# Optimization experiments

Hardware: AMD Instinct MI355X
Metric: run time of the kernel (lower is better)

## Reference

```python
import jax, jax.numpy as jnp
import numpy as np

D = 32      # bond_dim
N = 784     # 28*28 physical sites
HALF = 392  # single_rank = rank // 2
L = 10      # labels
B = 128     # batch


def setup_inputs() -> dict:
    key = jax.random.key(0)
    k0, k1, k2, k3, k4, k5 = jax.random.split(key, 6)
    # per-site 2-component input features; components sum to 1 so the
    # 392-step transfer-matrix product stays numerically stable in fp32
    u = jax.random.uniform(k0, (B, N), dtype=jnp.float32)
    x = jnp.stack([u, 1.0 - u], axis=-1)  # (B, 784, 2)

    eye = jnp.eye(D, dtype=jnp.float32)[None, :, None, :]  # (1, D, 1, D)
    a0 = jax.random.normal(k1, (D, 2), dtype=jnp.float32) / np.float32(np.sqrt(D))
    cores_left = eye + 0.01 * jax.random.normal(k2, (HALF - 1, D, 2, D), dtype=jnp.float32)
    core_mid = 0.05 * jax.random.normal(k3, (D, L, D), dtype=jnp.float32)
    cores_right = eye + 0.01 * jax.random.normal(k4, (HALF - 1, D, 2, D), dtype=jnp.float32)
    a_end = jax.random.normal(k5, (D, 2), dtype=jnp.float32) / np.float32(np.sqrt(D))
    return {"x": x, "a0": a0, "cores_left": cores_left, "core_mid": core_mid,
            "cores_right": cores_right, "a_end": a_end}


def reference(x, a0, cores_left, core_mid, cores_right, a_end):
    # ---- left half: nodes 0..391 contracted with inputs 0..391 ----
    v0 = jnp.einsum('dp,bp->bd', a0, x[:, 0])                       # (B, D)
    # input-contracted transfer matrices for nodes 1..391
    Ml = jnp.einsum('nlpr,bnp->nblr', cores_left, x[:, 1:HALF])      # (391, B, D, D)

    def step_left(c, M):
        return jnp.einsum('bl,blr->br', c, M), None

    left, _ = jax.lax.scan(step_left, v0, Ml)                        # (B, D)

    # ---- right half: nodes 393..784 contracted with inputs 392..783 ----
    r0 = jnp.einsum('dp,bp->bd', a_end, x[:, N - 1])                 # (B, D)
    Mr = jnp.einsum('nlpr,bnp->nblr', cores_right, x[:, HALF:N - 1])  # (391, B, D, D)

    def step_right(c, M):
        return jnp.einsum('blr,br->bl', M, c), None

    right, _ = jax.lax.scan(step_right, r0, Mr, reverse=True)        # (B, D)

    # ---- middle label node: original does einsum('a,aba,a->b') (diagonal!) ----
    mid_diag = jnp.einsum('aba->ab', core_mid)                       # (D, L)
    return jnp.einsum('ba,ba,ac->bc', left, right, mid_diag)         # (B, 10)
```

## Files before the change

### kernel.cpp

```cpp
#include <hip/hip_runtime.h>

#define NSTEP 391
#define NB 128

typedef __attribute__((ext_vector_type(8))) short s8v;
typedef __attribute__((ext_vector_type(16))) float f32x16;

typedef const __attribute__((address_space(1))) void* gas_ptr;
typedef __attribute__((address_space(3))) void* las_ptr;

union I4S8 { int4 i; s8v v; };
union W4S8 { int w[4]; s8v v; };

#define WAITVM(N) do { asm volatile("s_waitcnt vmcnt(" #N ")" ::: "memory"); \
                       __builtin_amdgcn_sched_barrier(0); } while (0)
#define LGKM0     do { asm volatile("s_waitcnt lgkmcnt(0)" ::: "memory");   \
                       __builtin_amdgcn_sched_barrier(0); } while (0)
#define SBAR      do { __builtin_amdgcn_s_barrier();                        \
                       __builtin_amdgcn_sched_barrier(0); } while (0)

__device__ __forceinline__ int pack_hi(float a, float b) {
    return (__float_as_int(b) & 0xffff0000) | ((unsigned)__float_as_int(a) >> 16);
}
__device__ __forceinline__ float trunc_bf(float a) {
    return __int_as_float(__float_as_int(a) & 0xffff0000);
}
__device__ __forceinline__ int cvtpk(float a, float b) {
    int r;
    asm("v_cvt_pk_bf16_f32 %0, %1, %2" : "=v"(r) : "v"(a), "v"(b));
    return r;
}

__global__ __launch_bounds__(256) void prep(
    const float* __restrict__ coresL, const float* __restrict__ coresR,
    int* __restrict__ aprep) {
    const int bid = blockIdx.x;
    const int side = bid >= NSTEP;
    const int t = bid - side * NSTEP;
    const float* st = (side ? coresR : coresL) + t * 2048;
    int* out = aprep + (size_t)(side * NSTEP + t) * 2048;
    for (int o = threadIdx.x; o < 2048; o += 256) {
        const int f = o >> 8, lane = (o >> 2) & 63, w = o & 3;
        const int part = f >> 2, p = (f >> 1) & 1, j = f & 1;
        const int h = lane >> 5, c = lane & 31;
        const int k0 = j * 16 + h * 8 + w * 2;
        float e0, e1;
        if (!side) { e0 = st[c * 64 + p * 32 + k0];  e1 = st[c * 64 + p * 32 + k0 + 1]; }
        else       { e0 = st[k0 * 64 + p * 32 + c];  e1 = st[(k0 + 1) * 64 + p * 32 + c]; }
        out[o] = (part == 0) ? pack_hi(e0, e1)
                             : pack_hi(e0 - trunc_bf(e0), e1 - trunc_bf(e1));
    }
}

__device__ __forceinline__ void bpack(const float* d, bool h0, W4S8& b1h, W4S8& b2h,
                                      W4S8& b1l, W4S8& b2l) {
#if __has_builtin(__builtin_amdgcn_permlane32_swap)
    int hw[8], lw[8];
    #pragma unroll
    for (int q = 0; q < 8; ++q) {
        float e = d[2 * q], o = d[2 * q + 1];
        hw[q] = __builtin_amdgcn_perm(__float_as_uint(o), __float_as_uint(e), 0x07060302u);
        lw[q] = cvtpk(e - trunc_bf(e), o - trunc_bf(o));
    }
    {
        auto r0 = __builtin_amdgcn_permlane32_swap(hw[0], hw[2], false, false);
        b1h.w[0] = r0[0]; b1h.w[2] = r0[1];
        auto r1 = __builtin_amdgcn_permlane32_swap(hw[1], hw[3], false, false);
        b1h.w[1] = r1[0]; b1h.w[3] = r1[1];
        auto r2 = __builtin_amdgcn_permlane32_swap(hw[4], hw[6], false, false);
        b2h.w[0] = r2[0]; b2h.w[2] = r2[1];
        auto r3 = __builtin_amdgcn_permlane32_swap(hw[5], hw[7], false, false);
        b2h.w[1] = r3[0]; b2h.w[3] = r3[1];
        auto r4 = __builtin_amdgcn_permlane32_swap(lw[0], lw[2], false, false);
        b1l.w[0] = r4[0]; b1l.w[2] = r4[1];
        auto r5 = __builtin_amdgcn_permlane32_swap(lw[1], lw[3], false, false);
        b1l.w[1] = r5[0]; b1l.w[3] = r5[1];
        auto r6 = __builtin_amdgcn_permlane32_swap(lw[4], lw[6], false, false);
        b2l.w[0] = r6[0]; b2l.w[2] = r6[1];
        auto r7 = __builtin_amdgcn_permlane32_swap(lw[5], lw[7], false, false);
        b2l.w[1] = r7[0]; b2l.w[3] = r7[1];
    }
    (void)h0;
#else
    float sx[16];
    #pragma unroll
    for (int r = 0; r < 16; ++r) sx[r] = __shfl_xor(d[r], 32);
    float B1[8], B2[8];
    #pragma unroll
    for (int m = 0; m < 4; ++m) {
        B1[m]     = h0 ? d[m]      : sx[4 + m];
        B1[4 + m] = h0 ? sx[m]     : d[4 + m];
        B2[m]     = h0 ? d[8 + m]  : sx[12 + m];
        B2[4 + m] = h0 ? sx[8 + m] : d[12 + m];
    }
    #pragma unroll
    for (int ww = 0; ww < 4; ++ww) {
        b1h.w[ww] = pack_hi(B1[2 * ww], B1[2 * ww + 1]);
        b2h.w[ww] = pack_hi(B2[2 * ww], B2[2 * ww + 1]);
        b1l.w[ww] = cvtpk(B1[2 * ww] - trunc_bf(B1[2 * ww]),
                          B1[2 * ww + 1] - trunc_bf(B1[2 * ww + 1]));
        b2l.w[ww] = cvtpk(B2[2 * ww] - trunc_bf(B2[2 * ww]),
                          B2[2 * ww + 1] - trunc_bf(B2[2 * ww + 1]));
    }
#endif
}

__device__ __forceinline__ void mstep(float* d, const I4S8* fr,
                                      const W4S8& b1h, const W4S8& b2h,
                                      const W4S8& b1l, const W4S8& b2l, float2 xv) {
    f32x16 acc0 = {}; f32x16 acc1 = {};
    acc0 = __builtin_amdgcn_mfma_f32_32x32x16_bf16(fr[0].v, b1h.v, acc0, 0, 0, 0);
    acc1 = __builtin_amdgcn_mfma_f32_32x32x16_bf16(fr[2].v, b1h.v, acc1, 0, 0, 0);
    acc0 = __builtin_amdgcn_mfma_f32_32x32x16_bf16(fr[1].v, b2h.v, acc0, 0, 0, 0);
    acc1 = __builtin_amdgcn_mfma_f32_32x32x16_bf16(fr[3].v, b2h.v, acc1, 0, 0, 0);
    acc0 = __builtin_amdgcn_mfma_f32_32x32x16_bf16(fr[0].v, b1l.v, acc0, 0, 0, 0);
    acc1 = __builtin_amdgcn_mfma_f32_32x32x16_bf16(fr[2].v, b1l.v, acc1, 0, 0, 0);
    acc0 = __builtin_amdgcn_mfma_f32_32x32x16_bf16(fr[1].v, b2l.v, acc0, 0, 0, 0);
    acc1 = __builtin_amdgcn_mfma_f32_32x32x16_bf16(fr[3].v, b2l.v, acc1, 0, 0, 0);
    acc0 = __builtin_amdgcn_mfma_f32_32x32x16_bf16(fr[4].v, b1h.v, acc0, 0, 0, 0);
    acc1 = __builtin_amdgcn_mfma_f32_32x32x16_bf16(fr[6].v, b1h.v, acc1, 0, 0, 0);
    acc0 = __builtin_amdgcn_mfma_f32_32x32x16_bf16(fr[5].v, b2h.v, acc0, 0, 0, 0);
    acc1 = __builtin_amdgcn_mfma_f32_32x32x16_bf16(fr[7].v, b2h.v, acc1, 0, 0, 0);
    #pragma unroll
    for (int r = 0; r < 16; ++r) d[r] = fmaf(xv.y, acc1[r], xv.x * acc0[r]);
}

__device__ __forceinline__ void issue_part(const int* tb, int* slot, int lane, int wv) {
    const int f0 = wv * 2;
    __builtin_amdgcn_global_load_lds((gas_ptr)(tb + f0 * 256 + lane * 4),
                                     (las_ptr)(slot + f0 * 256), 16, 0, 0);
    __builtin_amdgcn_global_load_lds((gas_ptr)(tb + (f0 + 1) * 256 + lane * 4),
                                     (las_ptr)(slot + (f0 + 1) * 256), 16, 0, 0);
}

template <int NG>
__global__ __launch_bounds__(256, 4) void stage1(
    const float* __restrict__ x, const int* __restrict__ aprep,
    float* __restrict__ qws) {
    __shared__ int ring[2][2048];
    __shared__ float2 xls[8][16];
    const int wv = threadIdx.x >> 6;
    const int lane = threadIdx.x & 63;
    constexpr int SPX = 2 * NG / 8;
    const int dsp = blockIdx.x;
    const int xcd = dsp & 7;
    const int s = dsp >> 3;
    const int stream = xcd + 8 * (s % SPX);
    const int inb = s / SPX;
    const int side = stream >= NG;
    const int g = stream & (NG - 1);
    const int b0 = inb * 8 + wv * 2;
    constexpr int qq = NSTEP / NG, rr = NSTEP % NG;
    const int a = g * qq + (g < rr ? g : rr);
    const int len = qq + (g < rr ? 1 : 0);
    const int h = lane >> 5, col = lane & 31;
    const bool h0 = (h == 0);

    {
        const int u = lane >> 5, ll = lane & 31;
        if (ll < len) {
            int t = side ? (392 + a + ll) : (a + len - ll);
            xls[wv * 2 + u][ll] = ((const float2*)x + (b0 + u) * 784)[t];
        }
    }

    float dA[16], dB[16];
    #pragma unroll
    for (int r = 0; r < 16; ++r) {
        float iv = (((r & 3) + 8 * (r >> 2) + 4 * h) == col) ? 1.0f : 0.0f;
        dA[r] = iv; dB[r] = iv;
    }

    const int* tbase = aprep + (size_t)side * NSTEP * 2048;
    auto taddr = [&](int j) {
        int t = side ? (a + j) : (a + len - 1 - j);
        t = t < 0 ? 0 : (t > NSTEP - 1 ? NSTEP - 1 : t);
        return tbase + (size_t)t * 2048;
    };

    issue_part(taddr(0), ring[0], lane, wv);
    issue_part(taddr(1), ring[1], lane, wv);

    for (int j = 0; j < len; ++j) {
        int* slot = ring[j & 1];
        W4S8 p1h, p2h, p1l, p2l, q1h, q2h, q1l, q2l;
        bpack(dA, h0, p1h, p2h, p1l, p2l);
        bpack(dB, h0, q1h, q2h, q1l, q2l);
        WAITVM(2);
        SBAR;
        I4S8 fr[8];
        #pragma unroll
        for (int f = 0; f < 8; ++f)
            fr[f].i = *(const int4*)(slot + f * 256 + lane * 4);
        LGKM0;
        SBAR;
        issue_part(taddr(j + 2), slot, lane, wv);
        mstep(dA, fr, p1h, p2h, p1l, p2l, xls[wv * 2][j]);
        mstep(dB, fr, q1h, q2h, q1l, q2l, xls[wv * 2 + 1][j]);
    }
    WAITVM(0);

    float4* q0 = (float4*)(qws + ((size_t)(side * NB + b0) * NG + g) * 1024 + lane * 16);
    float4* q1 = (float4*)(qws + ((size_t)(side * NB + b0 + 1) * NG + g) * 1024 + lane * 16);
    q0[0] = make_float4(dA[0], dA[1], dA[2], dA[3]);
    q0[1] = make_float4(dA[4], dA[5], dA[6], dA[7]);
    q0[2] = make_float4(dA[8], dA[9], dA[10], dA[11]);
    q0[3] = make_float4(dA[12], dA[13], dA[14], dA[15]);
    q1[0] = make_float4(dB[0], dB[1], dB[2], dB[3]);
    q1[1] = make_float4(dB[4], dB[5], dB[6], dB[7]);
    q1[2] = make_float4(dB[8], dB[9], dB[10], dB[11]);
    q1[3] = make_float4(dB[12], dB[13], dB[14], dB[15]);
}

template <int NG>
__global__ __launch_bounds__(64) void stage2f(
    const float* __restrict__ x, const float* __restrict__ a0,
    const float* __restrict__ aend, const float* __restrict__ qws,
    const float* __restrict__ mid, float* __restrict__ out) {
    __shared__ float ring[2][2048];
    const int b = blockIdx.x;
    const int lane = threadIdx.x;
    const int c = lane & 31;
    const int j = lane >> 5;
    const float2* xb = (const float2*)x + b * 784;
    float2 x0 = xb[0], xe = xb[783];
    float v0 = fmaf(a0[c * 2], x0.x, a0[c * 2 + 1] * x0.y);
    float v1 = fmaf(aend[c * 2], xe.x, aend[c * 2 + 1] * xe.y);

    auto issue = [&](int i, float* slot) {
        int ic = i < NG - 1 ? i : NG - 1;
        const float* t0 = qws + ((size_t)b * NG + ic) * 1024;
        const float* t1 = qws + ((size_t)(NB + b) * NG + (NG - 1 - ic)) * 1024;
        #pragma unroll
        for (int u = 0; u < 4; ++u) {
            __builtin_amdgcn_global_load_lds((gas_ptr)(t0 + u * 256 + lane * 4),
                                             (las_ptr)(slot + u * 256), 16, 0, 0);
            __builtin_amdgcn_global_load_lds((gas_ptr)(t1 + u * 256 + lane * 4),
                                             (las_ptr)(slot + 1024 + u * 256), 16, 0, 0);
        }
    };
    issue(0, ring[0]);
    issue(1, ring[1]);

    for (int i = 0; i < NG; ++i) {
        float* slot = ring[i & 1];
        WAITVM(8);
        float q0[16], q1[16];
        #pragma unroll
        for (int u = 0; u < 4; ++u) {
            float4 t4 = *(const float4*)(slot + lane * 16 + u * 4);
            q0[4 * u] = t4.x; q0[4 * u + 1] = t4.y; q0[4 * u + 2] = t4.z; q0[4 * u + 3] = t4.w;
            float4 t5 = *(const float4*)(slot + 1024 + lane * 16 + u * 4);
            q1[4 * u] = t5.x; q1[4 * u + 1] = t5.y; q1[4 * u + 2] = t5.z; q1[4 * u + 3] = t5.w;
        }
        LGKM0;
        issue(i + 2, slot);
        float s0 = 0.f, s1 = 0.f, s2 = 0.f, s3 = 0.f;
        float u0 = 0.f, u1 = 0.f, u2 = 0.f, u3 = 0.f;
        #pragma unroll
        for (int r = 0; r < 16; r += 4) {
            const int base = 8 * (r >> 2) + 4 * j;
            s0 = fmaf(__shfl(v0, base + 0, 64), q0[r + 0], s0);
            u0 = fmaf(__shfl(v1, base + 0, 64), q1[r + 0], u0);
            s1 = fmaf(__shfl(v0, base + 1, 64), q0[r + 1], s1);
            u1 = fmaf(__shfl(v1, base + 1, 64), q1[r + 1], u1);
            s2 = fmaf(__shfl(v0, base + 2, 64), q0[r + 2], s2);
            u2 = fmaf(__shfl(v1, base + 2, 64), q1[r + 2], u2);
            s3 = fmaf(__shfl(v0, base + 3, 64), q0[r + 3], s3);
            u3 = fmaf(__shfl(v1, base + 3, 64), q1[r + 3], u3);
        }
        float sv = (s0 + s1) + (s2 + s3);
        float uv = (u0 + u1) + (u2 + u3);
        sv += __shfl_xor(sv, 32);
        uv += __shfl_xor(uv, 32);
        v0 = sv; v1 = uv;
    }
    WAITVM(0);

    float pa = v0 * v1;
    #pragma unroll
    for (int cc = 0; cc < 10; ++cc) {
        float s = pa * mid[c * 320 + cc * 32 + c];
        s += __shfl_xor(s, 16, 32);
        s += __shfl_xor(s, 8, 32);
        s += __shfl_xor(s, 4, 32);
        s += __shfl_xor(s, 2, 32);
        s += __shfl_xor(s, 1, 32);
        if (lane == 0) out[b * 10 + cc] = s;
    }
}

extern "C" void kernel_launch(void* const* d_in, const int* in_sizes, int n_in,
                              void* d_out, int out_size, void* d_ws, size_t ws_size,
                              hipStream_t stream) {
    const float* x      = (const float*)d_in[0];
    const float* a0     = (const float*)d_in[1];
    const float* coresL = (const float*)d_in[2];
    const float* mid    = (const float*)d_in[3];
    const float* coresR = (const float*)d_in[4];
    const float* aend   = (const float*)d_in[5];

    int*   aprep = (int*)d_ws;
    float* qws   = (float*)d_ws + 2 * NSTEP * 2048;
    float* out   = (float*)d_out;

    const size_t need32 = (size_t)(2 * NSTEP * 2048) * 4
                        + (size_t)2 * NB * 32 * 1024 * 4;

    prep<<<dim3(2 * NSTEP), dim3(256), 0, stream>>>(coresL, coresR, aprep);
    if (ws_size >= need32) {
        stage1<32><<<dim3(1024), dim3(256), 0, stream>>>(x, aprep, qws);
        stage2f<32><<<dim3(NB), dim3(64), 0, stream>>>(x, a0, aend, qws, mid, out);
    } else {
        stage1<16><<<dim3(512), dim3(256), 0, stream>>>(x, aprep, qws);
        stage2f<16><<<dim3(NB), dim3(64), 0, stream>>>(x, a0, aend, qws, mid, out);
    }
}
```

Measured before the change: 73.67 us.

## Software-pipeline stage1 with per-wave full tile loads and register double-buffering

Each wave now issues the global-to-LDS loads for the whole 8-fragment transfer-matrix tile itself, rather than splitting it across the four waves. This lets every wave wait only on its own vmcnt and drops one block barrier per step. Fragments for the next step are read from LDS into a second register set while the MFMAs for the current step run. The loop is unrolled by two and the MFMA section is raised with s_setprio. The cost is four times the global/L2 load traffic, since all waves fetch the same tile, plus higher register pressure; the x staging buffer is also enlarged.

```diff
diff --git a/kernel.cpp b/kernel.cpp
--- a/kernel.cpp
+++ b/kernel.cpp
@@ -18,6 +18,7 @@
                        __builtin_amdgcn_sched_barrier(0); } while (0)
 #define SBAR      do { __builtin_amdgcn_s_barrier();                        \
                        __builtin_amdgcn_sched_barrier(0); } while (0)
+#define SCHED0    __builtin_amdgcn_sched_barrier(0)
 
 __device__ __forceinline__ int pack_hi(float a, float b) {
     return (__float_as_int(b) & 0xffff0000) | ((unsigned)__float_as_int(a) >> 16);
@@ -125,12 +126,17 @@
     for (int r = 0; r < 16; ++r) d[r] = fmaf(xv.y, acc1[r], xv.x * acc0[r]);
 }
 
-__device__ __forceinline__ void issue_part(const int* tb, int* slot, int lane, int wv) {
-    const int f0 = wv * 2;
-    __builtin_amdgcn_global_load_lds((gas_ptr)(tb + f0 * 256 + lane * 4),
-                                     (las_ptr)(slot + f0 * 256), 16, 0, 0);
-    __builtin_amdgcn_global_load_lds((gas_ptr)(tb + (f0 + 1) * 256 + lane * 4),
-                                     (las_ptr)(slot + (f0 + 1) * 256), 16, 0, 0);
+__device__ __forceinline__ void issue_full(const int* tb, int* slot, int lane) {
+    #pragma unroll
+    for (int f = 0; f < 8; ++f)
+        __builtin_amdgcn_global_load_lds((gas_ptr)(tb + f * 256 + lane * 4),
+                                         (las_ptr)(slot + f * 256), 16, 0, 0);
+}
+
+__device__ __forceinline__ void ldfr(I4S8* fr, const int* slot, int lane) {
+    #pragma unroll
+    for (int f = 0; f < 8; ++f)
+        fr[f].i = *(const int4*)(slot + f * 256 + lane * 4);
 }
 
 template <int NG>
@@ -138,7 +144,7 @@
     const float* __restrict__ x, const int* __restrict__ aprep,
     float* __restrict__ qws) {
     __shared__ int ring[2][2048];
-    __shared__ float2 xls[8][16];
+    __shared__ float2 xls[8][28];
     const int wv = threadIdx.x >> 6;
     const int lane = threadIdx.x & 63;
     constexpr int SPX = 2 * NG / 8;
@@ -178,26 +184,36 @@
         return tbase + (size_t)t * 2048;
     };
 
-    issue_part(taddr(0), ring[0], lane, wv);
-    issue_part(taddr(1), ring[1], lane, wv);
-
-    for (int j = 0; j < len; ++j) {
-        int* slot = ring[j & 1];
-        W4S8 p1h, p2h, p1l, p2l, q1h, q2h, q1l, q2l;
-        bpack(dA, h0, p1h, p2h, p1l, p2l);
-        bpack(dB, h0, q1h, q2h, q1l, q2l);
-        WAITVM(2);
-        SBAR;
-        I4S8 fr[8];
-        #pragma unroll
-        for (int f = 0; f < 8; ++f)
-            fr[f].i = *(const int4*)(slot + f * 256 + lane * 4);
-        LGKM0;
-        SBAR;
-        issue_part(taddr(j + 2), slot, lane, wv);
-        mstep(dA, fr, p1h, p2h, p1l, p2l, xls[wv * 2][j]);
-        mstep(dB, fr, q1h, q2h, q1l, q2l, xls[wv * 2 + 1][j]);
-    }
+    I4S8 frA[8], frB[8];
+    issue_full(taddr(0), ring[0], lane);
+    issue_full(taddr(1), ring[1], lane);
+    WAITVM(8);
+    ldfr(frA, ring[0], lane);
+
+    #define STEP1(j, frC, frN)                                               \
+    {                                                                        \
+        LGKM0;                          \
+        SBAR;                 \
+        issue_full(taddr((j) + 2), ring[(j) & 1], lane);                     \
+        W4S8 p1h, p2h, p1l, p2l, q1h, q2h, q1l, q2l;                         \
+        bpack(dA, h0, p1h, p2h, p1l, p2l);                                   \
+        bpack(dB, h0, q1h, q2h, q1l, q2l);                                   \
+        WAITVM(8);     \
+        ldfr(frN, ring[((j) + 1) & 1], lane);                                \
+        SCHED0;        \
+        __builtin_amdgcn_s_setprio(1);                                       \
+        mstep(dA, frC, p1h, p2h, p1l, p2l, xls[wv * 2][j]);                  \
+        mstep(dB, frC, q1h, q2h, q1l, q2l, xls[wv * 2 + 1][j]);              \
+        __builtin_amdgcn_s_setprio(0);                                       \
+    }
+
+    int j = 0;
+    for (; j + 2 <= len; j += 2) {
+        STEP1(j, frA, frB);
+        STEP1(j + 1, frB, frA);
+    }
+    if (j < len) STEP1(j, frA, frB);
+    #undef STEP1
     WAITVM(0);
 
     float4* q0 = (float4*)(qws + ((size_t)(side * NB + b0) * NG + g) * 1024 + lane * 16);
```

Measured after the change: 90.34 us. +22.6%, slower.
